# Kernel tuning notes

Measured on AMD Instinct MI355X. Metric: run time of the kernel, lower is better.

The kernel has to match this reference:

```python
import jax, jax.numpy as jnp
import numpy as np

D = 64          # d_in
NH = [256, 256] # nn_depth_design
L = 16          # flow_layers
B = 32768       # batch of samples


def _build_masks():
    # Deterministic mask maps: this_min=0, this_max=d_in-1 for all layers
    mh0 = np.arange(NH[0]) % (D - 1)
    mh1 = np.arange(NH[1]) % (D - 1)
    M1 = (mh0[None, :] <= mh1[:, None]).astype(np.float32)  # [nh1, nh0]
    M0s, M2s = [], []
    for l in range(L):
        perm = np.arange(D) if l % 2 == 0 else np.arange(D)[::-1]
        M0s.append((perm[None, :] <= mh0[:, None]).astype(np.float32))  # [nh0, D]
        M2s.append((mh1[None, :] < perm[:, None]).astype(np.float32))  # [D, nh1]
    M0 = np.stack(M0s)                                   # [L, nh0, D]
    M1 = np.broadcast_to(M1, (L,) + M1.shape).copy()     # [L, nh1, nh0]
    M2 = np.stack(M2s)                                   # [L, D, nh1]
    return jnp.asarray(M0), jnp.asarray(M1), jnp.asarray(M2)


def setup_inputs() -> dict:
    key = jax.random.key(0)
    ks = jax.random.split(key, 13)
    u = jax.random.normal(ks[0], (B, D), dtype=jnp.float32)

    def w(k, shape, fan_in):
        return jax.random.uniform(k, shape, jnp.float32, -1.0, 1.0) / np.sqrt(fan_in)

    inp = {"u": u}
    i = 1
    for net in ("loc", "scale"):
        inp[f"{net}_W0"] = w(ks[i], (L, NH[0], D), D); i += 1
        inp[f"{net}_b0"] = w(ks[i], (L, NH[0]), D); i += 1
        inp[f"{net}_W1"] = w(ks[i], (L, NH[1], NH[0]), NH[0]); i += 1
        inp[f"{net}_b1"] = w(ks[i], (L, NH[1]), NH[0]); i += 1
        inp[f"{net}_W2"] = w(ks[i], (L, D, NH[1]), NH[1]); i += 1
        inp[f"{net}_b2"] = w(ks[i], (L, D), NH[1]); i += 1
    M0, M1, M2 = _build_masks()
    inp["M0"], inp["M1"], inp["M2"] = M0, M1, M2
    return inp


def reference(u, loc_W0, loc_b0, loc_W1, loc_b1, loc_W2, loc_b2,
              scale_W0, scale_b0, scale_W1, scale_b1, scale_W2, scale_b2,
              M0, M1, M2):
    def step(y, p):
        (lW0, lb0, lW1, lb1, lW2, lb2,
         sW0, sb0, sW1, sb1, sW2, sb2, m0, m1, m2) = p

        def net(W0, b0, W1, b1, W2, b2):
            h = jax.nn.relu(y @ (m0 * W0).T + b0)    # [B, nh0]
            h = jax.nn.relu(h @ (m1 * W1).T + b1)    # [B, nh1]
            return h @ (m2 * W2).T + b2              # [B, D]

        loc = net(lW0, lb0, lW1, lb1, lW2, lb2)
        sc = net(sW0, sb0, sW1, sb1, sW2, sb2)
        # inverse=False coupling: exp(-scale) * (y - loc)
        return jnp.exp(-sc) * (y - loc), None

    params = (loc_W0, loc_b0, loc_W1, loc_b1, loc_W2, loc_b2,
              scale_W0, scale_b0, scale_W1, scale_b1, scale_W2, scale_b2,
              M0, M1, M2)
    y, _ = jax.lax.scan(step, u, params)
    return y
```

## Files before the change

### kernel.cpp

```cpp
#include <hip/hip_runtime.h>
#include <hip/hip_bf16.h>

typedef __bf16 bf16x8 __attribute__((ext_vector_type(8)));
typedef __bf16 bf16x4 __attribute__((ext_vector_type(4)));
typedef float  f32x4  __attribute__((ext_vector_type(4)));

#define LAYERS 16
#define DIM 64
#define NHID 256
#define BATCH 32768
#define MTILE 64
#define NBLOCKS (BATCH / MTILE)

#define W0P_PER 16384
#define W1P_PER 65536
#define W2P_PER 16384
#define W0P_TOT (32 * W0P_PER)
#define W1P_TOT (32 * W1P_PER)
#define W2P_TOT (32 * W2P_PER)
#define PACK_TOT (W0P_TOT + W1P_TOT + W2P_TOT)

__device__ __forceinline__ bf16x8 ldw(const __bf16* p) { return *(const bf16x8*)p; }

__global__ __launch_bounds__(256) void pack_weights(
    const float* __restrict__ lW0, const float* __restrict__ lW1, const float* __restrict__ lW2,
    const float* __restrict__ sW0, const float* __restrict__ sW1, const float* __restrict__ sW2,
    __bf16* __restrict__ ws)
{
    const long i = ((long)blockIdx.x * 256 + threadIdx.x) * 8;
    const float* W; long src; int l, n, k, which;
    if (i < W0P_TOT) {
        int netl = (int)(i / W0P_PER), rem = (int)(i % W0P_PER);
        int net = netl >> 4; l = netl & 15;
        int nt = rem >> 10, kt = (rem >> 9) & 1, lane = (rem >> 3) & 63;
        n = nt * 16 + (lane & 15); k = kt * 32 + (lane >> 4) * 8;
        W = net ? sW0 : lW0; which = 0;
        src = (long)(l * 256 + n) * 64 + k;
    } else if (i < W0P_TOT + W1P_TOT) {
        long r = i - W0P_TOT;
        int netl = (int)(r / W1P_PER), rem = (int)(r % W1P_PER);
        int net = netl >> 4; l = netl & 15;
        int nt = rem >> 12, kt = (rem >> 9) & 7, lane = (rem >> 3) & 63;
        n = nt * 16 + (lane & 15); k = kt * 32 + (lane >> 4) * 8;
        W = net ? sW1 : lW1; which = 1;
        src = (long)(l * 256 + n) * 256 + k;
    } else {
        long r = i - W0P_TOT - W1P_TOT;
        int netl = (int)(r / W2P_PER), rem = (int)(r % W2P_PER);
        int net = netl >> 4; l = netl & 15;
        int nt = rem >> 12, kt = (rem >> 9) & 7, lane = (rem >> 3) & 63;
        n = nt * 16 + (lane & 15); k = kt * 32 + (lane >> 4) * 8;
        W = net ? sW2 : lW2; which = 2;
        src = (long)(l * 64 + n) * 256 + k;
    }
    f32x4 wa = *(const f32x4*)(W + src);
    f32x4 wb = *(const f32x4*)(W + src + 4);
    const int nm = n % 63;
    const int pn = (l & 1) ? 63 - n : n;
    bf16x8 o;
    #pragma unroll
    for (int j = 0; j < 8; ++j) {
        int kk = k + j;
        bool m;
        if (which == 0)      { int pk = (l & 1) ? 63 - kk : kk; m = (pk <= nm); }
        else if (which == 1) { m = ((kk % 63) <= nm); }
        else                 { m = ((kk % 63) < pn); }
        float v = (j < 4) ? wa[j] : wb[j - 4];
        o[j] = m ? (__bf16)v : (__bf16)0.0f;
    }
    *(bf16x8*)(ws + i) = o;
}

__global__ void __launch_bounds__(512, 4)
flow_kernel(
    const float* __restrict__ u,
    const __bf16* __restrict__ wp,
    const float* __restrict__ lb0, const float* __restrict__ lb1, const float* __restrict__ lb2,
    const float* __restrict__ sb0, const float* __restrict__ sb1, const float* __restrict__ sb2,
    float* __restrict__ out)
{
    __shared__ __bf16 ybf[4 * 2 * 512];
    __shared__ __bf16 buf1[4 * 8 * 512];
    __shared__ __bf16 buf2[4 * 8 * 512];

    const int tid  = threadIdx.x;
    const int w    = tid >> 6;
    const int lane = tid & 63;
    const int quad = lane >> 4;
    const int l16  = lane & 15;
    const int blk  = blockIdx.x;

    const int qh = quad >> 1;
    const int qp = (quad & 1) * 4;

    const int otD = w >> 1;
    const int bh  = w & 1;

    const __bf16* w0p = wp;
    const __bf16* w1p = wp + W0P_TOT;
    const __bf16* w2p = wp + W0P_TOT + W1P_TOT;

    f32x4 y[2];
    #pragma unroll
    for (int bt = 0; bt < 2; ++bt)
        y[bt] = *(const f32x4*)(u + (long)(blk * MTILE + bh * 32 + bt * 16 + l16) * DIM
                                  + otD * 16 + quad * 4);

    const int ktY = w >> 2;
    const int flY = ((((w >> 1) & 1) * 2 + qh) * 16 + l16);

    bf16x8 wg1[4];
    #pragma unroll
    for (int oi = 0; oi < 2; ++oi)
        #pragma unroll
        for (int kt = 0; kt < 2; ++kt)
            wg1[oi * 2 + kt] = ldw(w0p + (long)((2 * w + oi) * 2 + kt) * 512 + lane * 8);

    for (int l = 0; l < LAYERS; ++l) {
        #pragma unroll
        for (int bt = 0; bt < 2; ++bt) {
            bf16x4 v;
            #pragma unroll
            for (int r = 0; r < 4; ++r) v[r] = (__bf16)y[bt][r];
            *(bf16x4*)&ybf[(((bh * 2 + bt) * 2 + ktY) * 64 + flY) * 8 + qp] = v;
        }
        __syncthreads();

        f32x4 locr[2], scr[2];

        #pragma unroll
        for (int net = 0; net < 2; ++net) {
            const __bf16* w1b = w1p + (long)(net * 16 + l) * W1P_PER;
            const __bf16* w2b = w2p + (long)(net * 16 + l) * W2P_PER;
            const __bf16* w0n = w0p + (long)(net == 0 ? 16 + l : l + 1) * W0P_PER;
            const float* b0 = (net ? sb0 : lb0) + l * 256;
            const float* b1 = (net ? sb1 : lb1) + l * 256;
            const float* b2 = (net ? sb2 : lb2) + l * 64;

            bf16x8 wg2a[8];

            {
                f32x4 acc[2][4];
                #pragma unroll
                for (int oi = 0; oi < 2; ++oi)
                    #pragma unroll
                    for (int bt = 0; bt < 4; ++bt)
                        acc[oi][bt] = (f32x4){0.f, 0.f, 0.f, 0.f};
                #pragma unroll
                for (int kt = 0; kt < 2; ++kt) {
                    bf16x8 bv[4];
                    #pragma unroll
                    for (int bt = 0; bt < 4; ++bt)
                        bv[bt] = *(const bf16x8*)&ybf[((bt * 2 + kt) * 64 + lane) * 8];
                    #pragma unroll
                    for (int oi = 0; oi < 2; ++oi)
                        #pragma unroll
                        for (int bt = 0; bt < 4; ++bt)
                            acc[oi][bt] = __builtin_amdgcn_mfma_f32_16x16x32_bf16(wg1[oi * 2 + kt], bv[bt], acc[oi][bt], 0, 0, 0);
                }
                #pragma unroll
                for (int kt = 0; kt < 4; ++kt)
                    #pragma unroll
                    for (int oi = 0; oi < 2; ++oi)
                        wg2a[kt * 2 + oi] = ldw(w1b + (long)((2 * w + oi) * 8 + kt) * 512 + lane * 8);
                #pragma unroll
                for (int oi = 0; oi < 2; ++oi) {
                    f32x4 bias = *(const f32x4*)(b0 + (2 * w + oi) * 16 + quad * 4);
                    const int fl = ((oi * 2 + qh) * 16 + l16);
                    #pragma unroll
                    for (int bt = 0; bt < 4; ++bt) {
                        bf16x4 v;
                        #pragma unroll
                        for (int r = 0; r < 4; ++r)
                            v[r] = (__bf16)fmaxf(acc[oi][bt][r] + bias[r], 0.f);
                        *(bf16x4*)&buf1[((bt * 8 + w) * 64 + fl) * 8 + qp] = v;
                    }
                }
            }
            __syncthreads();

            bf16x8 wg3[8];

            {
                f32x4 acc[2][4];
                #pragma unroll
                for (int oi = 0; oi < 2; ++oi)
                    #pragma unroll
                    for (int bt = 0; bt < 4; ++bt)
                        acc[oi][bt] = (f32x4){0.f, 0.f, 0.f, 0.f};
                #pragma unroll
                for (int kt = 0; kt < 8; ++kt) {
                    bf16x8 aw[2];
                    #pragma unroll
                    for (int oi = 0; oi < 2; ++oi)
                        aw[oi] = (kt < 4) ? wg2a[kt * 2 + oi]
                                          : ldw(w1b + (long)((2 * w + oi) * 8 + kt) * 512 + lane * 8);
                    bf16x8 bv[4];
                    #pragma unroll
                    for (int bt = 0; bt < 4; ++bt)
                        bv[bt] = *(const bf16x8*)&buf1[((bt * 8 + kt) * 64 + lane) * 8];
                    #pragma unroll
                    for (int oi = 0; oi < 2; ++oi)
                        #pragma unroll
                        for (int bt = 0; bt < 4; ++bt)
                            acc[oi][bt] = __builtin_amdgcn_mfma_f32_16x16x32_bf16(aw[oi], bv[bt], acc[oi][bt], 0, 0, 0);
                }
                #pragma unroll
                for (int oi = 0; oi < 2; ++oi) {
                    f32x4 bias = *(const f32x4*)(b1 + (2 * w + oi) * 16 + quad * 4);
                    const int fl = ((oi * 2 + qh) * 16 + l16);
                    #pragma unroll
                    for (int bt = 0; bt < 4; ++bt) {
                        bf16x4 v;
                        #pragma unroll
                        for (int r = 0; r < 4; ++r)
                            v[r] = (__bf16)fmaxf(acc[oi][bt][r] + bias[r], 0.f);
                        *(bf16x4*)&buf2[((bt * 8 + w) * 64 + fl) * 8 + qp] = v;
                    }
                }
                #pragma unroll
                for (int kt = 0; kt < 8; ++kt)
                    wg3[kt] = ldw(w2b + (long)(otD * 8 + kt) * 512 + lane * 8);
            }
            __syncthreads();

            {
                f32x4 acc3[2];
                #pragma unroll
                for (int bt = 0; bt < 2; ++bt)
                    acc3[bt] = (f32x4){0.f, 0.f, 0.f, 0.f};
                #pragma unroll
                for (int kt = 0; kt < 8; ++kt) {
                    #pragma unroll
                    for (int bt = 0; bt < 2; ++bt) {
                        bf16x8 bv = *(const bf16x8*)&buf2[(((bh * 2 + bt) * 8 + kt) * 64 + lane) * 8];
                        acc3[bt] = __builtin_amdgcn_mfma_f32_16x16x32_bf16(wg3[kt], bv, acc3[bt], 0, 0, 0);
                    }
                }
                #pragma unroll
                for (int oi = 0; oi < 2; ++oi)
                    #pragma unroll
                    for (int kt = 0; kt < 2; ++kt)
                        wg1[oi * 2 + kt] = ldw(w0n + (long)((2 * w + oi) * 2 + kt) * 512 + lane * 8);
                f32x4 bias = *(const f32x4*)(b2 + otD * 16 + quad * 4);
                if (net == 0) {
                    #pragma unroll
                    for (int bt = 0; bt < 2; ++bt)
                        #pragma unroll
                        for (int r = 0; r < 4; ++r)
                            locr[bt][r] = acc3[bt][r] + bias[r];
                } else {
                    #pragma unroll
                    for (int bt = 0; bt < 2; ++bt)
                        #pragma unroll
                        for (int r = 0; r < 4; ++r)
                            scr[bt][r] = acc3[bt][r] + bias[r];
                }
            }
        }

        #pragma unroll
        for (int bt = 0; bt < 2; ++bt)
            #pragma unroll
            for (int r = 0; r < 4; ++r)
                y[bt][r] = __expf(-scr[bt][r]) * (y[bt][r] - locr[bt][r]);
    }

    #pragma unroll
    for (int bt = 0; bt < 2; ++bt)
        *(f32x4*)(out + (long)(blk * MTILE + bh * 32 + bt * 16 + l16) * DIM
                      + otD * 16 + quad * 4) = y[bt];
}

extern "C" void kernel_launch(void* const* d_in, const int* in_sizes, int n_in,
                              void* d_out, int out_size, void* d_ws, size_t ws_size,
                              hipStream_t stream) {
    const float* u   = (const float*)d_in[0];
    const float* lW0 = (const float*)d_in[1];
    const float* lb0 = (const float*)d_in[2];
    const float* lW1 = (const float*)d_in[3];
    const float* lb1 = (const float*)d_in[4];
    const float* lW2 = (const float*)d_in[5];
    const float* lb2 = (const float*)d_in[6];
    const float* sW0 = (const float*)d_in[7];
    const float* sb0 = (const float*)d_in[8];
    const float* sW1 = (const float*)d_in[9];
    const float* sb1 = (const float*)d_in[10];
    const float* sW2 = (const float*)d_in[11];
    const float* sb2 = (const float*)d_in[12];

    if (ws_size < (size_t)PACK_TOT * sizeof(__bf16)) return;
    __bf16* ws = (__bf16*)d_ws;

    pack_weights<<<PACK_TOT / 8 / 256, 256, 0, stream>>>(
        lW0, lW1, lW2, sW0, sW1, sW2, ws);
    flow_kernel<<<NBLOCKS, 512, 0, stream>>>(
        u, ws, lb0, lb1, lb2, sb0, sb1, sb2, (float*)d_out);
}
```

Measured before the change: 299.7 us.

## Repartition hidden-layer GEMM work so each wave owns a batch half and more outputs

Changes the wave-to-tile mapping of the first two hidden-layer GEMMs. Each wave now computes 4 output tiles (64 hidden units) for 32 batch rows instead of 2 output tiles for all 64 rows. This halves the LDS B-operand reads per wave and matches the batch-half ownership of the final layer. In exchange, every wave must load twice as much weight data from global memory and hold more weight registers, which may raise register pressure and lower occupancy.

```diff
diff --git a/kernel.cpp b/kernel.cpp
--- a/kernel.cpp
+++ b/kernel.cpp
@@ -109,12 +109,12 @@
     const int ktY = w >> 2;
     const int flY = ((((w >> 1) & 1) * 2 + qh) * 16 + l16);
 
-    bf16x8 wg1[4];
+    bf16x8 wg1[8];
     #pragma unroll
-    for (int oi = 0; oi < 2; ++oi)
+    for (int oi = 0; oi < 4; ++oi)
         #pragma unroll
         for (int kt = 0; kt < 2; ++kt)
-            wg1[oi * 2 + kt] = ldw(w0p + (long)((2 * w + oi) * 2 + kt) * 512 + lane * 8);
+            wg1[oi * 2 + kt] = ldw(w0p + (long)((4 * otD + oi) * 2 + kt) * 512 + lane * 8);
 
     for (int l = 0; l < LAYERS; ++l) {
         #pragma unroll
@@ -137,43 +137,45 @@
             const float* b1 = (net ? sb1 : lb1) + l * 256;
             const float* b2 = (net ? sb2 : lb2) + l * 64;
 
-            bf16x8 wg2a[8];
+            bf16x8 wg2a[16];
 
             {
-                f32x4 acc[2][4];
-                #pragma unroll
-                for (int oi = 0; oi < 2; ++oi)
-                    #pragma unroll
-                    for (int bt = 0; bt < 4; ++bt)
-                        acc[oi][bt] = (f32x4){0.f, 0.f, 0.f, 0.f};
+                f32x4 acc[4][2];
+                #pragma unroll
+                for (int oi = 0; oi < 4; ++oi)
+                    #pragma unroll
+                    for (int bl = 0; bl < 2; ++bl)
+                        acc[oi][bl] = (f32x4){0.f, 0.f, 0.f, 0.f};
                 #pragma unroll
                 for (int kt = 0; kt < 2; ++kt) {
-                    bf16x8 bv[4];
-                    #pragma unroll
-                    for (int bt = 0; bt < 4; ++bt)
-                        bv[bt] = *(const bf16x8*)&ybf[((bt * 2 + kt) * 64 + lane) * 8];
-                    #pragma unroll
-                    for (int oi = 0; oi < 2; ++oi)
-                        #pragma unroll
-                        for (int bt = 0; bt < 4; ++bt)
-                            acc[oi][bt] = __builtin_amdgcn_mfma_f32_16x16x32_bf16(wg1[oi * 2 + kt], bv[bt], acc[oi][bt], 0, 0, 0);
+                    bf16x8 bv[2];
+                    #pragma unroll
+                    for (int bl = 0; bl < 2; ++bl)
+                        bv[bl] = *(const bf16x8*)&ybf[(((2 * bh + bl) * 2 + kt) * 64 + lane) * 8];
+                    #pragma unroll
+                    for (int oi = 0; oi < 4; ++oi)
+                        #pragma unroll
+                        for (int bl = 0; bl < 2; ++bl)
+                            acc[oi][bl] = __builtin_amdgcn_mfma_f32_16x16x32_bf16(wg1[oi * 2 + kt], bv[bl], acc[oi][bl], 0, 0, 0);
                 }
                 #pragma unroll
                 for (int kt = 0; kt < 4; ++kt)
                     #pragma unroll
-                    for (int oi = 0; oi < 2; ++oi)
-                        wg2a[kt * 2 + oi] = ldw(w1b + (long)((2 * w + oi) * 8 + kt) * 512 + lane * 8);
-                #pragma unroll
-                for (int oi = 0; oi < 2; ++oi) {
-                    f32x4 bias = *(const f32x4*)(b0 + (2 * w + oi) * 16 + quad * 4);
-                    const int fl = ((oi * 2 + qh) * 16 + l16);
-                    #pragma unroll
-                    for (int bt = 0; bt < 4; ++bt) {
+                    for (int oi = 0; oi < 4; ++oi)
+                        wg2a[kt * 4 + oi] = ldw(w1b + (long)((4 * otD + oi) * 8 + kt) * 512 + lane * 8);
+                #pragma unroll
+                for (int oi = 0; oi < 4; ++oi) {
+                    const int O = 4 * otD + oi;
+                    f32x4 bias = *(const f32x4*)(b0 + O * 16 + quad * 4);
+                    const int kt1 = O >> 1;
+                    const int fl  = ((O & 1) * 2 + qh) * 16 + l16;
+                    #pragma unroll
+                    for (int bl = 0; bl < 2; ++bl) {
                         bf16x4 v;
                         #pragma unroll
                         for (int r = 0; r < 4; ++r)
-                            v[r] = (__bf16)fmaxf(acc[oi][bt][r] + bias[r], 0.f);
-                        *(bf16x4*)&buf1[((bt * 8 + w) * 64 + fl) * 8 + qp] = v;
+                            v[r] = (__bf16)fmaxf(acc[oi][bl][r] + bias[r], 0.f);
+                        *(bf16x4*)&buf1[(((2 * bh + bl) * 8 + kt1) * 64 + fl) * 8 + qp] = v;
                     }
                 }
             }
@@ -182,40 +184,42 @@
             bf16x8 wg3[8];
 
             {
-                f32x4 acc[2][4];
-                #pragma unroll
-                for (int oi = 0; oi < 2; ++oi)
-                    #pragma unroll
-                    for (int bt = 0; bt < 4; ++bt)
-                        acc[oi][bt] = (f32x4){0.f, 0.f, 0.f, 0.f};
+                f32x4 acc[4][2];
+                #pragma unroll
+                for (int oi = 0; oi < 4; ++oi)
+                    #pragma unroll
+                    for (int bl = 0; bl < 2; ++bl)
+                        acc[oi][bl] = (f32x4){0.f, 0.f, 0.f, 0.f};
                 #pragma unroll
                 for (int kt = 0; kt < 8; ++kt) {
-                    bf16x8 aw[2];
-                    #pragma unroll
-                    for (int oi = 0; oi < 2; ++oi)
-                        aw[oi] = (kt < 4) ? wg2a[kt * 2 + oi]
-                                          : ldw(w1b + (long)((2 * w + oi) * 8 + kt) * 512 + lane * 8);
-                    bf16x8 bv[4];
-                    #pragma unroll
-                    for (int bt = 0; bt < 4; ++bt)
-                        bv[bt] = *(const bf16x8*)&buf1[((bt * 8 + kt) * 64 + lane) * 8];
-                    #pragma unroll
-                    for (int oi = 0; oi < 2; ++oi)
-                        #pragma unroll
-                        for (int bt = 0; bt < 4; ++bt)
-                            acc[oi][bt] = __builtin_amdgcn_mfma_f32_16x16x32_bf16(aw[oi], bv[bt], acc[oi][bt], 0, 0, 0);
-                }
-                #pragma unroll
-                for (int oi = 0; oi < 2; ++oi) {
-                    f32x4 bias = *(const f32x4*)(b1 + (2 * w + oi) * 16 + quad * 4);
-                    const int fl = ((oi * 2 + qh) * 16 + l16);
-                    #pragma unroll
-                    for (int bt = 0; bt < 4; ++bt) {
+                    bf16x8 aw[4];
+                    #pragma unroll
+                    for (int oi = 0; oi < 4; ++oi)
+                        aw[oi] = (kt < 4) ? wg2a[kt * 4 + oi]
+                                          : ldw(w1b + (long)((4 * otD + oi) * 8 + kt) * 512 + lane * 8);
+                    bf16x8 bv[2];
+                    #pragma unroll
+                    for (int bl = 0; bl < 2; ++bl)
+                        bv[bl] = *(const bf16x8*)&buf1[(((2 * bh + bl) * 8 + kt) * 64 + lane) * 8];
+                    #pragma unroll
+                    for (int oi = 0; oi < 4; ++oi)
+                        #pragma unroll
+                        for (int bl = 0; bl < 2; ++bl)
+                            acc[oi][bl] = __builtin_amdgcn_mfma_f32_16x16x32_bf16(aw[oi], bv[bl], acc[oi][bl], 0, 0, 0);
+                }
+                #pragma unroll
+                for (int oi = 0; oi < 4; ++oi) {
+                    const int O = 4 * otD + oi;
+                    f32x4 bias = *(const f32x4*)(b1 + O * 16 + quad * 4);
+                    const int kt1 = O >> 1;
+                    const int fl  = ((O & 1) * 2 + qh) * 16 + l16;
+                    #pragma unroll
+                    for (int bl = 0; bl < 2; ++bl) {
                         bf16x4 v;
                         #pragma unroll
                         for (int r = 0; r < 4; ++r)
-                            v[r] = (__bf16)fmaxf(acc[oi][bt][r] + bias[r], 0.f);
-                        *(bf16x4*)&buf2[((bt * 8 + w) * 64 + fl) * 8 + qp] = v;
+                            v[r] = (__bf16)fmaxf(acc[oi][bl][r] + bias[r], 0.f);
+                        *(bf16x4*)&buf2[(((2 * bh + bl) * 8 + kt1) * 64 + fl) * 8 + qp] = v;
                     }
                 }
                 #pragma unroll
@@ -238,10 +242,10 @@
                     }
                 }
                 #pragma unroll
-                for (int oi = 0; oi < 2; ++oi)
+                for (int oi = 0; oi < 4; ++oi)
                     #pragma unroll
                     for (int kt = 0; kt < 2; ++kt)
-                        wg1[oi * 2 + kt] = ldw(w0n + (long)((2 * w + oi) * 2 + kt) * 512 + lane * 8);
+                        wg1[oi * 2 + kt] = ldw(w0n + (long)((4 * otD + oi) * 2 + kt) * 512 + lane * 8);
                 f32x4 bias = *(const f32x4*)(b2 + otD * 16 + quad * 4);
                 if (net == 0) {
                     #pragma unroll
```

Result: slower. 559.2 us (+86.6%).
